# Kernel optimization log

Hardware: AMD Instinct MI355X
Metric: run time of the kernel (lower is better)

The kernel has to match this reference:

```python
import jax, jax.numpy as jnp
import numpy as np

HEAD_DIM = 128
NUM_HEADS = 16
HIDDEN = 2048
SEQ = 4096
ROPE_THETA = 10000.0
RMS_EPS = 1e-6


def _rms_norm(x, w, eps=RMS_EPS):
    # per-head RMSNorm over last dim (head_dim)
    var = jnp.mean(jnp.square(x), axis=-1, keepdims=True)
    return x * jax.lax.rsqrt(var + eps) * w


def _rope_cos_sin(position_ids, dim=HEAD_DIM, theta=ROPE_THETA):
    freqs = 1.0 / theta ** (jnp.arange(0, dim, 2, dtype=jnp.float32) / dim)  # [dim/2]
    ang = position_ids.astype(jnp.float32)[:, None] * freqs[None, :]  # [S, dim/2]
    return jnp.cos(ang), jnp.sin(ang)


def _apply_rope(x, cos, sin):
    # x: [S, H, D]; pairs (x0, x1) along last dim act as complex numbers
    S, H, D = x.shape
    xr = x.astype(jnp.float32).reshape(S, H, D // 2, 2)
    x0, x1 = xr[..., 0], xr[..., 1]
    c = cos[:, None, :]  # [S, 1, D/2]
    s = sin[:, None, :]
    o0 = x0 * c - x1 * s
    o1 = x0 * s + x1 * c
    out = jnp.stack((o0, o1), axis=-1).reshape(S, H, D)
    return out.astype(x.dtype)


def setup_inputs() -> dict:
    key = jax.random.key(0)
    ks = jax.random.split(key, 8)
    std = 0.02
    return {
        "hidden_states": jax.random.normal(ks[0], (SEQ, HIDDEN), dtype=jnp.float32),
        "position_ids": jnp.arange(SEQ, dtype=jnp.int64 if jax.config.jax_enable_x64 else jnp.int32),
        "wq": jax.random.normal(ks[1], (HIDDEN, HIDDEN), dtype=jnp.float32) * std,
        "wk": jax.random.normal(ks[2], (HIDDEN, HIDDEN), dtype=jnp.float32) * std,
        "wv": jax.random.normal(ks[3], (HIDDEN, HIDDEN), dtype=jnp.float32) * std,
        "wo": jax.random.normal(ks[4], (HIDDEN, HIDDEN), dtype=jnp.float32) * std,
        "q_norm_w": jnp.ones((HEAD_DIM,), dtype=jnp.float32),
        "k_norm_w": jnp.ones((HEAD_DIM,), dtype=jnp.float32),
    }


def reference(hidden_states, position_ids, wq, wk, wv, wo, q_norm_w, k_norm_w):
    S = hidden_states.shape[0]
    # QKV projections (NormalLinear: x @ weight)
    xq = hidden_states @ wq
    xk = hidden_states @ wk
    xv = hidden_states @ wv
    # split heads: [S, H, D]
    xq = xq.reshape(S, NUM_HEADS, HEAD_DIM)
    xk = xk.reshape(S, NUM_HEADS, HEAD_DIM)
    xv = xv.reshape(S, NUM_HEADS, HEAD_DIM)
    # per-head qk RMSNorm
    xq = _rms_norm(xq, q_norm_w)
    xk = _rms_norm(xk, k_norm_w)
    # rotary embedding
    cos, sin = _rope_cos_sin(position_ids)
    xq = _apply_rope(xq, cos, sin)
    xk = _apply_rope(xk, cos, sin)
    # scaled dot-product attention (no mask), TNH layout
    context = jax.nn.dot_product_attention(xq, xk, xv)
    # merge heads and output projection (dropout p=0 -> identity)
    out = context.reshape(S, NUM_HEADS * HEAD_DIM) @ wo
    return out
```

## Files before the change

kernel.cpp:

```cpp
#include <hip/hip_runtime.h>

typedef __bf16 bf16x8 __attribute__((ext_vector_type(8)));
typedef __bf16 bf16x4 __attribute__((ext_vector_type(4)));
typedef float  f32x4  __attribute__((ext_vector_type(4)));
typedef float  f32x16 __attribute__((ext_vector_type(16)));
typedef unsigned u32x4 __attribute__((ext_vector_type(4)));

#define MFMA16(A, B, C) __builtin_amdgcn_mfma_f32_16x16x32_bf16(A, B, C, 0, 0, 0)
#define MFMA32(A, B, C) __builtin_amdgcn_mfma_f32_32x32x16_bf16(A, B, C, 0, 0, 0)
#define AS1 __attribute__((address_space(1)))
#define AS3 __attribute__((address_space(3)))

#if __has_builtin(__builtin_amdgcn_exp2f)
#define EXP2F(x) __builtin_amdgcn_exp2f(x)
#else
#define EXP2F(x) exp2f(x)
#endif

__device__ __forceinline__ unsigned pk_bf16(float lo, float hi) {
    unsigned r;
    asm("v_cvt_pk_bf16_f32 %0, %1, %2" : "=v"(r) : "v"(lo), "v"(hi));
    return r;
}

__global__ __launch_bounds__(256) void prep(const float* __restrict__ hs,
                                            const float* __restrict__ wq,
                                            const float* __restrict__ wk,
                                            const float* __restrict__ wv,
                                            const float* __restrict__ wo,
                                            __bf16* __restrict__ xb,
                                            __bf16* __restrict__ wqkvtb,
                                            __bf16* __restrict__ wotb) {
    __shared__ float tl[64][65];
    const int z = blockIdx.z;
    const int t = threadIdx.x;
    if (z == 4) {
        size_t bid = (size_t)blockIdx.y * 32 + blockIdx.x;
        size_t base = bid * 8192 + (size_t)t * 4;
        for (int c = 0; c < 8; ++c) {
            float4 v = *(const float4*)(hs + base + c * 1024);
            bf16x4 o;
            o.x = (__bf16)v.x; o.y = (__bf16)v.y; o.z = (__bf16)v.z; o.w = (__bf16)v.w;
            *(bf16x4*)(xb + base + c * 1024) = o;
        }
        return;
    }
    const float* src = (z == 0) ? wq : (z == 1) ? wk : (z == 2) ? wv : wo;
    __bf16* dst = (z < 3) ? (wqkvtb + (size_t)z * 2048 * 2048) : wotb;
    int x0 = blockIdx.x * 64, y0 = blockIdx.y * 64;
    #pragma unroll
    for (int sw = 0; sw < 4; ++sw) {
        int r  = (t >> 4) + sw * 16;
        int c4 = (t & 15) * 4;
        float4 v = *(const float4*)&src[(size_t)(y0 + r) * 2048 + x0 + c4];
        tl[r][c4] = v.x; tl[r][c4 + 1] = v.y; tl[r][c4 + 2] = v.z; tl[r][c4 + 3] = v.w;
    }
    __syncthreads();
    #pragma unroll
    for (int sw = 0; sw < 2; ++sw) {
        int o  = (t >> 3) + sw * 32;
        int ch = t & 7;
        bf16x8 pk;
        #pragma unroll
        for (int j = 0; j < 8; ++j) pk[j] = (__bf16)tl[ch * 8 + j][o];
        *(bf16x8*)&dst[(size_t)(x0 + o) * 2048 + y0 + ch * 8] = pk;
    }
}

__global__ __launch_bounds__(256) void rope_vt(const __bf16* __restrict__ qkv,
                                               const float* __restrict__ qw,
                                               const float* __restrict__ kw,
                                               const int* __restrict__ pos_ids,
                                               __bf16* __restrict__ qhb,
                                               __bf16* __restrict__ khb,
                                               __bf16* __restrict__ vtb) {
    __shared__ __bf16 tl2[64][68];
    if (blockIdx.y < 32) {
        int u = threadIdx.x >> 6, lane = threadIdx.x & 63;
        int s = blockIdx.x * 4 + u;
        int slot = blockIdx.y;
        bool isQ = slot < 16;
        int h = slot & 15;
        size_t base = (size_t)s * 6144 + (isQ ? 0 : 2048) + h * 128 + lane * 2;
        float x0 = (float)qkv[base], x1 = (float)qkv[base + 1];
        float ss = x0 * x0 + x1 * x1;
        for (int m = 1; m < 64; m <<= 1) ss += __shfl_xor(ss, m);
        float rr = rsqrtf(ss * (1.0f / 128.0f) + 1e-6f);
        const float* wp = isQ ? qw : kw;
        float n0 = x0 * rr * wp[lane * 2], n1 = x1 * rr * wp[lane * 2 + 1];
        float freq = EXP2F(-(float)lane * 0.2076205059004571f);
        float ang = (float)pos_ids[s] * freq;
        float sn, cs;
        sincosf(ang, &sn, &cs);
        float o0 = n0 * cs - n1 * sn;
        float o1 = n0 * sn + n1 * cs;
        if (isQ) { o0 *= 0.12751744416196178f; o1 *= 0.12751744416196178f; }
        __bf16* dst = (isQ ? qhb : khb) + (size_t)h * 4096 * 128 + (size_t)s * 128 + lane * 2;
        dst[0] = (__bf16)o0; dst[1] = (__bf16)o1;
    } else {
        int linear = (blockIdx.y - 32) * 1024 + blockIdx.x;
        int h = linear >> 7, rem = linear & 127;
        int s0 = (rem & 63) * 64, d0 = (rem >> 6) * 64;
        int t = threadIdx.x;
        #pragma unroll
        for (int sw = 0; sw < 2; ++sw) {
            int sr = (t >> 3) + sw * 32;
            int ch = t & 7;
            uint4 v = *(const uint4*)&qkv[(size_t)(s0 + sr) * 6144 + 4096 + h * 128 + d0 + ch * 8];
            uint2 lo, hi;
            lo.x = v.x; lo.y = v.y; hi.x = v.z; hi.y = v.w;
            *(uint2*)&tl2[sr][ch * 8] = lo;
            *(uint2*)&tl2[sr][ch * 8 + 4] = hi;
        }
        __syncthreads();
        #pragma unroll
        for (int sw = 0; sw < 2; ++sw) {
            int o  = (t >> 3) + sw * 32;
            int ch = t & 7;
            bf16x8 pk;
            #pragma unroll
            for (int j = 0; j < 8; ++j) pk[j] = tl2[ch * 8 + j][o];
            *(bf16x8*)&vtb[(size_t)h * 128 * 4096 + (size_t)(d0 + o) * 4096 + s0 + ch * 8] = pk;
        }
    }
}

template <bool F32OUT>
__global__ __launch_bounds__(256) void gemm_bt(const __bf16* __restrict__ A, int lda,
                                               const __bf16* __restrict__ Bt, int ldb,
                                               void* __restrict__ Cout, int ldc, int K) {
    __shared__ __bf16 as[2][128][64];
    __shared__ __bf16 bs[2][128][64];
    const int m0 = blockIdx.x * 128, n0 = blockIdx.y * 128;
    const int t = threadIdx.x;
    const int lane = t & 63, w = t >> 6;
    const int wm = (w >> 1) * 64, wn = (w & 1) * 64;
    const int ln = lane & 15, quad = lane >> 4;
    auto as3 = (AS3 uint32_t*)&as[0][0][0];
    auto bs3 = (AS3 uint32_t*)&bs[0][0][0];
    const char* abase = (const char*)&as[0][0][0];
    const char* bbase = (const char*)&bs[0][0][0];
    const int scc = (t & 7) ^ ((t >> 3) & 7);
    f32x4 acc[4][4] = {};

#define G_STAGE(buf, k0)                                                             \
    for (int c = 0; c < 4; ++c) {                                                    \
        int g = c * 256 + t;                                                         \
        int row = g >> 3;                                                            \
        __builtin_amdgcn_global_load_lds(                                            \
            (const AS1 uint32_t*)&A[(size_t)(m0 + row) * lda + (k0) + scc * 8],      \
            as3 + (buf) * 4096 + g * 4, 16, 0, 0);                                   \
        __builtin_amdgcn_global_load_lds(                                            \
            (const AS1 uint32_t*)&Bt[(size_t)(n0 + row) * ldb + (k0) + scc * 8],     \
            bs3 + (buf) * 4096 + g * 4, 16, 0, 0);                                   \
    }

    const int nt = K >> 6;
    G_STAGE(0, 0)
    for (int kt = 0; kt < nt; ++kt) {
        if (kt + 1 < nt) {
            G_STAGE((kt + 1) & 1, (kt + 1) * 64)
            asm volatile("s_waitcnt vmcnt(8)" ::: "memory");
        } else {
            asm volatile("s_waitcnt vmcnt(0)" ::: "memory");
        }
        __builtin_amdgcn_s_barrier();
        const char* ab = abase + (kt & 1) * 16384;
        const char* bb = bbase + (kt & 1) * 16384;
        #pragma unroll
        for (int ks = 0; ks < 2; ++ks) {
            bf16x8 af[4], bfr[4];
            #pragma unroll
            for (int i = 0; i < 4; ++i) {
                int rr = wm + i * 16 + ln;
                af[i] = *(const bf16x8*)(ab + rr * 128 + (((ks * 4 + quad) ^ (ln & 7)) << 4));
            }
            #pragma unroll
            for (int j = 0; j < 4; ++j) {
                int rr = wn + j * 16 + ln;
                bfr[j] = *(const bf16x8*)(bb + rr * 128 + (((ks * 4 + quad) ^ (ln & 7)) << 4));
            }
            #pragma unroll
            for (int i = 0; i < 4; ++i)
                #pragma unroll
                for (int j = 0; j < 4; ++j)
                    acc[i][j] = MFMA16(af[i], bfr[j], acc[i][j]);
        }
        __builtin_amdgcn_s_barrier();
    }
#undef G_STAGE

    for (int i = 0; i < 4; ++i)
        for (int j = 0; j < 4; ++j)
            for (int r = 0; r < 4; ++r) {
                int row = m0 + wm + i * 16 + quad * 4 + r;
                int col = n0 + wn + j * 16 + ln;
                if (F32OUT) ((float*)Cout)[(size_t)row * ldc + col] = acc[i][j][r];
                else        ((__bf16*)Cout)[(size_t)row * ldc + col] = (__bf16)acc[i][j][r];
            }
}

#define SOFTMAX_PV(sac, ktv)                                                        \
    {                                                                               \
        float p[16];                                                                \
        _Pragma("unroll")                                                           \
        for (int r = 0; r < 16; ++r) { p[r] = EXP2F((sac)[r]); rs += p[r]; }        \
        unsigned a00 = pk_bf16(p[0], p[1]),  a01 = pk_bf16(p[2], p[3]);             \
        unsigned b00 = pk_bf16(p[4], p[5]),  b01 = pk_bf16(p[6], p[7]);             \
        unsigned a10 = pk_bf16(p[8], p[9]),  a11 = pk_bf16(p[10], p[11]);           \
        unsigned b10 = pk_bf16(p[12], p[13]), b11 = pk_bf16(p[14], p[15]);          \
        auto s00 = __builtin_amdgcn_permlane32_swap(a00, b00, false, false);        \
        auto s01 = __builtin_amdgcn_permlane32_swap(a01, b01, false, false);        \
        auto s10 = __builtin_amdgcn_permlane32_swap(a10, b10, false, false);        \
        auto s11 = __builtin_amdgcn_permlane32_swap(a11, b11, false, false);        \
        u32x4 w0, w1;                                                               \
        w0[0] = s00[0]; w0[1] = s01[0]; w0[2] = s00[1]; w0[3] = s01[1];             \
        w1[0] = s10[0]; w1[1] = s11[0]; w1[2] = s10[1]; w1[3] = s11[1];             \
        bf16x8 pf0 = __builtin_bit_cast(bf16x8, w0);                                \
        bf16x8 pf1 = __builtin_bit_cast(bf16x8, w1);                                \
        __builtin_amdgcn_s_setprio(1);                                              \
        _Pragma("unroll")                                                           \
        for (int dt = 0; dt < 4; ++dt) {                                            \
            int vrow = dt * 32 + q32;                                               \
            int co0 = (((ktv) * 2 + 0) << 1) | hi;                                  \
            int co1 = (((ktv) * 2 + 1) << 1) | hi;                                  \
            bf16x8 vf0 = *(const bf16x8*)(vsb + vrow * 128 + ((co0 ^ (q32 & 7)) << 4)); \
            bf16x8 vf1 = *(const bf16x8*)(vsb + vrow * 128 + ((co1 ^ (q32 & 7)) << 4)); \
            oacc[dt] = MFMA32(pf0, vf0, oacc[dt]);                                  \
            oacc[dt] = MFMA32(pf1, vf1, oacc[dt]);                                  \
        }                                                                           \
        __builtin_amdgcn_s_setprio(0);                                              \
    }

__global__ __launch_bounds__(256) void flash_attn(const __bf16* __restrict__ Q,
                                                  const __bf16* __restrict__ Kb,
                                                  const __bf16* __restrict__ Vt,
                                                  __bf16* __restrict__ ctx) {
    __shared__ __bf16 kbuf[2][64][128];
    __shared__ __bf16 vbuf[2][128][64];
    __shared__ float lred[4][32];

    int bid = blockIdx.x + (int)gridDim.x * blockIdx.y;
    int swz = (bid & 7) * 64 + (bid >> 3);
    const int h  = swz >> 5;
    const int m0 = (swz & 31) * 128;

    const int t = threadIdx.x;
    const int lane = t & 63, w = t >> 6;
    const int q32 = lane & 31, hi = lane >> 5;
    const __bf16* Qh = Q + (size_t)h * 4096 * 128;
    const __bf16* Kh = Kb + (size_t)h * 4096 * 128;
    const __bf16* Vh = Vt + (size_t)h * 128 * 4096;

    const int kcc = (t & 15) ^ ((t >> 4) & 7);
    const int vcc = (t & 7) ^ ((t >> 3) & 7);
    auto kb3 = (AS3 uint32_t*)&kbuf[0][0][0];
    auto vb3 = (AS3 uint32_t*)&vbuf[0][0][0];
    const char* kbase = (const char*)&kbuf[0][0][0];
    const char* vbase = (const char*)&vbuf[0][0][0];

    bf16x8 qf[8];
    for (int half = 0; half < 2; ++half) {
        for (int i = 0; i < 4; ++i) {
            int row = (t >> 4) + i * 16;
            *(uint4*)&kbuf[0][row][(t & 15) * 8] =
                *(const uint4*)&Qh[(size_t)(m0 + half * 64 + row) * 128 + kcc * 8];
        }
        __syncthreads();
        if ((w >> 1) == half) {
            int r = (w & 1) * 32 + q32;
            #pragma unroll
            for (int dc = 0; dc < 8; ++dc)
                qf[dc] = *(const bf16x8*)(kbase + r * 256 + ((((dc << 1) | hi) ^ (r & 7)) << 4));
        }
        __syncthreads();
    }

#define STAGE_KV(buf, tile)                                                          \
    for (int i = 0; i < 4; ++i) {                                                    \
        int krow = (t >> 4) + i * 16;                                                \
        __builtin_amdgcn_global_load_lds(                                            \
            (const AS1 uint32_t*)&Kh[(size_t)((tile) * 64 + krow) * 128 + kcc * 8],  \
            kb3 + (buf) * 4096 + (w * 64 + i * 256) * 4, 16, 0, 0);                  \
        int vrow = (t >> 3) + i * 32;                                                \
        __builtin_amdgcn_global_load_lds(                                            \
            (const AS1 uint32_t*)&Vh[(size_t)vrow * 4096 + (tile) * 64 + vcc * 8],   \
            vb3 + (buf) * 4096 + (w * 64 + i * 256) * 4, 16, 0, 0);                  \
    }

    STAGE_KV(0, 0)
    __syncthreads();

    f32x16 oacc[4] = {};
    float rs = 0.0f;
    int cur = 0;

    f32x16 mC16;
    #pragma unroll
    for (int e = 0; e < 16; ++e) mC16[e] = -16.5f;

    for (int kb = 0; kb < 64; ++kb) {
        if (kb + 1 < 64) { STAGE_KV(cur ^ 1, kb + 1) }

        const char* ksb = kbase + cur * 16384;
        const char* vsb = vbase + cur * 16384;

        f32x16 sacc0, sacc1;
        __builtin_amdgcn_s_setprio(1);
        {
            int co = hi;
            bf16x8 kf0 = *(const bf16x8*)(ksb + q32 * 256        + ((co ^ (q32 & 7)) << 4));
            bf16x8 kf1 = *(const bf16x8*)(ksb + (32 + q32) * 256 + ((co ^ (q32 & 7)) << 4));
            sacc0 = MFMA32(kf0, qf[0], mC16);
            sacc1 = MFMA32(kf1, qf[0], mC16);
        }
        #pragma unroll
        for (int dc = 1; dc < 8; ++dc) {
            int co = (dc << 1) | hi;
            bf16x8 kf0 = *(const bf16x8*)(ksb + q32 * 256        + ((co ^ (q32 & 7)) << 4));
            bf16x8 kf1 = *(const bf16x8*)(ksb + (32 + q32) * 256 + ((co ^ (q32 & 7)) << 4));
            sacc0 = MFMA32(kf0, qf[dc], sacc0);
            sacc1 = MFMA32(kf1, qf[dc], sacc1);
        }
        __builtin_amdgcn_s_setprio(0);

        SOFTMAX_PV(sacc0, 0)
        SOFTMAX_PV(sacc1, 1)

        __syncthreads();
        cur ^= 1;
    }
#undef STAGE_KV

    float rt = rs + __shfl_xor(rs, 32);
    if (hi == 0) lred[w][q32] = rt;
    __syncthreads();
    float inv[16];
    #pragma unroll
    for (int r = 0; r < 16; ++r)
        inv[r] = 1.0f / lred[w][(r & 3) + 8 * (r >> 2) + 4 * hi];
    #pragma unroll
    for (int dt = 0; dt < 4; ++dt)
        #pragma unroll
        for (int r = 0; r < 16; ++r) {
            int row = m0 + w * 32 + (r & 3) + 8 * (r >> 2) + 4 * hi;
            int col = h * 128 + dt * 32 + q32;
            ctx[(size_t)row * 2048 + col] = (__bf16)(oacc[dt][r] * inv[r]);
        }
}

extern "C" void kernel_launch(void* const* d_in, const int* in_sizes, int n_in,
                              void* d_out, int out_size, void* d_ws, size_t ws_size,
                              hipStream_t stream) {
    const float* hs  = (const float*)d_in[0];
    const int*   pos = (const int*)d_in[1];
    const float* wq  = (const float*)d_in[2];
    const float* wk  = (const float*)d_in[3];
    const float* wv  = (const float*)d_in[4];
    const float* wo  = (const float*)d_in[5];
    const float* qw  = (const float*)d_in[6];
    const float* kw  = (const float*)d_in[7];

    char* ws = (char*)d_ws;
    const size_t MB = 1024 * 1024;
    __bf16* xb     = (__bf16*)(ws + 0);
    __bf16* wqkvtb = (__bf16*)(ws + 16 * MB);
    __bf16* qhb    = (__bf16*)(ws + 0);
    __bf16* khb    = (__bf16*)(ws + 16 * MB);
    __bf16* vtb    = (__bf16*)(ws + 32 * MB);
    __bf16* qkvb   = (__bf16*)(ws + 48 * MB);
    __bf16* ctxb   = (__bf16*)(ws + 48 * MB);
    __bf16* wotb   = (__bf16*)(ws + 96 * MB);

    prep<<<dim3(32, 32, 5), 256, 0, stream>>>(hs, wq, wk, wv, wo, xb, wqkvtb, wotb);

    gemm_bt<false><<<dim3(32, 48), 256, 0, stream>>>(xb, 2048, wqkvtb, 2048, qkvb, 6144, 2048);

    rope_vt<<<dim3(1024, 34), 256, 0, stream>>>(qkvb, qw, kw, pos, qhb, khb, vtb);

    flash_attn<<<dim3(32, 16), 256, 0, stream>>>(qhb, khb, vtb, ctxb);

    gemm_bt<true><<<dim3(32, 16), 256, 0, stream>>>(ctxb, 2048, wotb, 2048, d_out, 2048, 2048);
}
```

Measured before the change: 455.4 us.

## Use 256x256-tile 512-thread GEMM with grid swizzle for QKV projection

Adds a new GEMM kernel for the fused QKV projection that uses 256x256 output tiles with 8 waves, double-buffered direct-to-LDS loads interleaved with the MFMA phases, s_setprio around the MFMA blocks, and a block-index swizzle for L2 locality. Larger tiles raise arithmetic intensity and cut global traffic per output element. In exchange it uses 128KB of LDS and many accumulator registers, which limits occupancy to one block per CU. The grid shrinks to 384 workgroups, which may leave some CUs underused.

```diff
diff --git a/kernel.cpp b/kernel.cpp
--- a/kernel.cpp
+++ b/kernel.cpp
@@ -125,6 +125,109 @@
     }
 }
 
+__global__ __launch_bounds__(512) void gemm256(const __bf16* __restrict__ A, int lda,
+                                               const __bf16* __restrict__ Bt, int ldb,
+                                               __bf16* __restrict__ Cout, int ldc, int K) {
+    __shared__ __bf16 as[2][256][64];
+    __shared__ __bf16 bs[2][256][64];
+    const int nwg = (int)(gridDim.x * gridDim.y);
+    const int bid = (int)(blockIdx.x + gridDim.x * blockIdx.y);
+    const int swz = (bid & 7) * (nwg >> 3) + (bid >> 3);
+    const int m0 = (swz % (int)gridDim.x) * 256;
+    const int n0 = (swz / (int)gridDim.x) * 256;
+    const int t = threadIdx.x;
+    const int lane = t & 63, w = t >> 6;
+    const int wm = (w >> 2) * 128, wn = (w & 3) * 64;
+    const int ln = lane & 15, quad = lane >> 4;
+    auto as3 = (AS3 uint32_t*)&as[0][0][0];
+    auto bs3 = (AS3 uint32_t*)&bs[0][0][0];
+    const char* abase = (const char*)&as[0][0][0];
+    const char* bbase = (const char*)&bs[0][0][0];
+    const int scc = (t & 7) ^ ((t >> 3) & 7);
+    f32x4 acc[8][4] = {};
+
+#define STG_A(buf, k0, l0)                                                           \
+    for (int l = (l0); l < (l0) + 2; ++l) {                                          \
+        int g = l * 512 + t;                                                         \
+        int row = g >> 3;                                                            \
+        __builtin_amdgcn_global_load_lds(                                            \
+            (const AS1 uint32_t*)&A[(size_t)(m0 + row) * lda + (k0) + scc * 8],      \
+            as3 + (buf) * 8192 + g * 4, 16, 0, 0);                                   \
+    }
+#define STG_B(buf, k0, l0)                                                           \
+    for (int l = (l0); l < (l0) + 2; ++l) {                                          \
+        int g = l * 512 + t;                                                         \
+        int row = g >> 3;                                                            \
+        __builtin_amdgcn_global_load_lds(                                            \
+            (const AS1 uint32_t*)&Bt[(size_t)(n0 + row) * ldb + (k0) + scc * 8],     \
+            bs3 + (buf) * 8192 + g * 4, 16, 0, 0);                                   \
+    }
+
+    const int nt = K >> 6;
+    STG_A(0, 0, 0) STG_A(0, 0, 2) STG_B(0, 0, 0) STG_B(0, 0, 2)
+
+    for (int kt = 0; kt < nt; ++kt) {
+        const int b = kt & 1;
+        const char* ab = abase + b * 32768;
+        const char* bb = bbase + b * 32768;
+        const int k1 = (kt + 1) * 64;
+        const bool pf = (kt + 1 < nt);
+
+        if (pf) { STG_A(b ^ 1, k1, 0) }
+        if (pf) asm volatile("s_waitcnt vmcnt(2)" ::: "memory");
+        else    asm volatile("s_waitcnt vmcnt(0)" ::: "memory");
+        __builtin_amdgcn_s_barrier();
+
+        #pragma unroll
+        for (int p = 0; p < 4; ++p) {
+            const int mh = p >> 1, nh = p & 1;
+            bf16x8 af[4][2], bf[2][2];
+            #pragma unroll
+            for (int i2 = 0; i2 < 4; ++i2) {
+                int rr = wm + (mh * 4 + i2) * 16 + ln;
+                #pragma unroll
+                for (int ks = 0; ks < 2; ++ks)
+                    af[i2][ks] = *(const bf16x8*)(ab + rr * 128 +
+                                                  (((ks * 4 + quad) ^ (ln & 7)) << 4));
+            }
+            #pragma unroll
+            for (int j2 = 0; j2 < 2; ++j2) {
+                int rn = wn + (nh * 2 + j2) * 16 + ln;
+                #pragma unroll
+                for (int ks = 0; ks < 2; ++ks)
+                    bf[j2][ks] = *(const bf16x8*)(bb + rn * 128 +
+                                                  (((ks * 4 + quad) ^ (ln & 7)) << 4));
+            }
+            if (pf) {
+                if (p == 0)      { STG_A(b ^ 1, k1, 2) }
+                else if (p == 1) { STG_B(b ^ 1, k1, 0) }
+                else if (p == 2) { STG_B(b ^ 1, k1, 2) }
+            }
+            __builtin_amdgcn_s_setprio(1);
+            #pragma unroll
+            for (int i2 = 0; i2 < 4; ++i2)
+                #pragma unroll
+                for (int j2 = 0; j2 < 2; ++j2)
+                    #pragma unroll
+                    for (int ks = 0; ks < 2; ++ks)
+                        acc[mh * 4 + i2][nh * 2 + j2] =
+                            MFMA16(af[i2][ks], bf[j2][ks], acc[mh * 4 + i2][nh * 2 + j2]);
+            __builtin_amdgcn_s_setprio(0);
+            __builtin_amdgcn_s_barrier();
+        }
+    }
+#undef STG_A
+#undef STG_B
+
+    for (int i = 0; i < 8; ++i)
+        for (int j = 0; j < 4; ++j)
+            for (int r = 0; r < 4; ++r) {
+                int row = m0 + wm + i * 16 + quad * 4 + r;
+                int col = n0 + wn + j * 16 + ln;
+                Cout[(size_t)row * ldc + col] = (__bf16)acc[i][j][r];
+            }
+}
+
 template <bool F32OUT>
 __global__ __launch_bounds__(256) void gemm_bt(const __bf16* __restrict__ A, int lda,
                                                const __bf16* __restrict__ Bt, int ldb,
@@ -374,7 +477,7 @@
 
     prep<<<dim3(32, 32, 5), 256, 0, stream>>>(hs, wq, wk, wv, wo, xb, wqkvtb, wotb);
 
-    gemm_bt<false><<<dim3(32, 48), 256, 0, stream>>>(xb, 2048, wqkvtb, 2048, qkvb, 6144, 2048);
+    gemm256<<<dim3(16, 24), 512, 0, stream>>>(xb, 2048, wqkvtb, 2048, qkvb, 6144, 2048);
 
     rope_vt<<<dim3(1024, 34), 256, 0, stream>>>(qkvb, qw, kw, pos, qhb, khb, vtb);
 
```

New measurement: 482.4 us. 5.9% more time.
